# Performance work log

Hardware: AMD Instinct MI355X
Metric: run time of the kernel (lower is better)

Reference implementation:

```python
import jax, jax.numpy as jnp
import numpy as np

EMBED_DIM = 512
BLOCK = 511
N_HEAD = 8
N_GLOBAL = 4
N_LOCAL = 2
N_MIX = 2
RECEP = 4
T = 2 * BLOCK + 2  # [task, clip, BLOCK upper, BLOCK lower]
HD = EMBED_DIM // N_HEAD
NEG = -1e9


def _build_masks():
    bs = BLOCK
    temporal = np.concatenate([np.zeros(2), np.arange(bs) * 2 + 1, np.arange(bs) * 2 + 2])
    seq = temporal[None, :] <= temporal[:, None]  # causal over interleaved temporal order
    tq = np.concatenate([np.arange(bs) * 2 + 1 - 2 * RECEP + 1] * 2)
    tk = np.concatenate([np.arange(bs) * 2 + 1] * 2)
    de = tk[None, :] < tq[:, None]  # keys too far in the past for the sliding window
    local = seq.copy()
    local[2:, 2:] = local[2:, 2:] & ~de
    return jnp.asarray(local), jnp.asarray(seq)


LOCAL_MASK, GLOBAL_MASK = _build_masks()  # (T, T) bool, True = visible


def _linear_params(key, fan_in, fan_out):
    k1, k2 = jax.random.split(key)
    s = 1.0 / np.sqrt(fan_in)
    W = jax.random.uniform(k1, (fan_out, fan_in), minval=-s, maxval=s, dtype=jnp.float32)
    b = jax.random.uniform(k2, (fan_out,), minval=-s, maxval=s, dtype=jnp.float32)
    return W, b


def setup_inputs() -> dict:
    key = jax.random.key(0)
    ks = jax.random.split(key, 10)
    B = 4
    x = jax.random.normal(ks[0], (B, T, EMBED_DIM), dtype=jnp.float32)
    cond_mask = jnp.ones((B, T), dtype=jnp.float32)
    Wq, bq = _linear_params(ks[1], EMBED_DIM, EMBED_DIM)
    Wk, bk = _linear_params(ks[2], EMBED_DIM, EMBED_DIM)
    Wv, bv = _linear_params(ks[3], EMBED_DIM, EMBED_DIM)
    Wqml, bqml = _linear_params(ks[4], EMBED_DIM, HD * N_MIX)
    Wkml, bkml = _linear_params(ks[5], EMBED_DIM, HD * N_MIX)
    Wp, bp = _linear_params(ks[6], EMBED_DIM, EMBED_DIM)
    mix_w = jax.random.normal(ks[7], (N_MIX, 2), dtype=jnp.float32) * 0.5  # Conv2d(2*nm, nm, groups=nm, 1x1)
    bias_clip = jnp.full((1, N_HEAD, 1), 0.5, dtype=jnp.float32)
    bias_clip_ml = jnp.full((1, N_MIX, 1), 0.5, dtype=jnp.float32)
    return dict(x=x, cond_mask=cond_mask, Wq=Wq, bq=bq, Wk=Wk, bk=bk, Wv=Wv, bv=bv,
                Wqml=Wqml, bqml=bqml, Wkml=Wkml, bkml=bkml, mix_w=mix_w, Wp=Wp, bp=bp,
                bias_clip=bias_clip, bias_clip_ml=bias_clip_ml)


def reference(x, cond_mask, Wq, bq, Wk, bk, Wv, bv, Wqml, bqml, Wkml, bkml, mix_w, Wp, bp, bias_clip, bias_clip_ml):
    B, Tx, C = x.shape

    def heads(W, b, nh):
        return (x @ W.T + b).reshape(B, Tx, nh, HD).transpose(0, 2, 1, 3)  # (B, nh, T, hd)

    q = heads(Wq, bq, N_HEAD)
    k = heads(Wk, bk, N_HEAD)
    v = heads(Wv, bv, N_HEAD)
    qml = heads(Wqml, bqml, N_MIX)
    kml = heads(Wkml, bkml, N_MIX)

    scale = 1.0 / np.sqrt(HD)
    # main attention: heads [0:N_LOCAL] local-masked, rest global (causal) masked
    att = jnp.einsum('bhqd,bhkd->bhqk', q, k) * scale
    att = att.at[:, :, :, 1].add(bias_clip)  # learned bias on the CLIP-token key column
    head_mask = jnp.concatenate([
        jnp.broadcast_to(LOCAL_MASK, (N_LOCAL, Tx, Tx)),
        jnp.broadcast_to(GLOBAL_MASK, (N_MIX + N_GLOBAL, Tx, Tx))], axis=0)
    att = jax.nn.softmax(jnp.where(head_mask[None], att, NEG), axis=-1)

    # extra local-masked score maps for the mix heads
    aml = jnp.einsum('bhqd,bhkd->bhqk', qml, kml) * scale
    aml = aml.at[:, :, :, 1].add(bias_clip_ml)
    aml = jax.nn.softmax(jnp.where(LOCAL_MASK[None, None], aml, NEG), axis=-1)

    # grouped 1x1 conv: per mix head, blend (global, local) attention maps
    mix_in = jnp.stack([att[:, N_LOCAL:N_LOCAL + N_MIX], aml], axis=2)  # (B, nm, 2, T, T)
    mix_out = jnp.einsum('ho,bhoqk->bhqk', mix_w, mix_in)

    att_f = jnp.concatenate([att[:, :N_LOCAL], mix_out, att[:, N_LOCAL + N_MIX:]], axis=1)
    y = jnp.einsum('bhqk,bhkd->bhqd', att_f, v)
    y = y.transpose(0, 2, 1, 3).reshape(B, Tx, C)
    return y @ Wp.T + bp
```

## Files before the change

kernel.cpp:

```cpp
#include <hip/hip_runtime.h>

typedef unsigned short u16;
typedef __attribute__((ext_vector_type(8))) __bf16 bf16x8;
typedef __attribute__((ext_vector_type(4))) float f32x4;
typedef __attribute__((ext_vector_type(8))) short short8;
typedef __attribute__((ext_vector_type(4))) u16 us4;
typedef __attribute__((ext_vector_type(4))) unsigned u32x4;

#define T_SEQ 1024
#define PW 1280
#define QSC 0.18033688f
#define L2E 1.4426950408889634f

__device__ __forceinline__ u16 f2bf(float f) {
  unsigned u = __float_as_uint(f);
  u += 0x7fff + ((u >> 16) & 1);
  return (u16)(u >> 16);
}
__device__ __forceinline__ float bf2f(u16 v) {
  return __uint_as_float((unsigned)v << 16);
}

__constant__ u16 GLOB_M[16] = {0x0101,0x0303,0x0707,0x0F0F,0x1F1F,0x3F3F,0x7F7F,0xFFFF,
                               0xFFFF,0x0307,0x070F,0x0F1F,0x1F3F,0x3F7F,0x7FFF,0xFFFF};
__constant__ u16 LOC_M[16]  = {0x0101,0x0303,0x0607,0x0C0D,0x1819,0x3031,0x6061,0xC0C1,
                               0x8183,0x0307,0x060F,0x0C1D,0x1839,0x3071,0x60E1,0xC1C1};

__device__ __forceinline__ void gll16(const u16* gp, u16* lp) {
  __builtin_amdgcn_global_load_lds((const __attribute__((address_space(1))) unsigned*)gp,
                                   (__attribute__((address_space(3))) unsigned*)lp, 16, 0, 0);
}

template<int NISS>
__device__ __forceinline__ void stage_sw(u16* lds, const u16* __restrict__ g,
                                         int ld, int tid) {
  const int w = tid >> 6;
#pragma unroll
  for (int i = 0; i < NISS; ++i) {
    int row = i * 32 + (tid >> 3);
    int cswz = ((tid & 7) << 4) ^ ((row & 7) << 4);
    gll16(g + (size_t)row * ld + (cswz >> 1), lds + i * 2048 + w * 512);
  }
}

__device__ __forceinline__ void stage8(u16* lds, const u16* __restrict__ g,
                                       int ld, int tid) {
  int row = tid >> 3;
  int cswz = (((tid & 7) << 4) ^ ((row & 7) << 4)) >> 1;
  gll16(g + (size_t)row * ld + cswz, lds + (tid >> 6) * 512);
}

__device__ __forceinline__ bf16x8 rd_sw(const u16* lds, int row, int colbyte) {
  return *(const bf16x8*)&lds[row * 64 + ((colbyte ^ ((row & 7) << 4)) >> 1)];
}

__global__ void prep_all(const float4* __restrict__ x, u16* __restrict__ xb,
                         const float* __restrict__ Wq, const float* __restrict__ Wk,
                         const float* __restrict__ Wv, const float* __restrict__ Wqml,
                         const float* __restrict__ Wkml, const float* __restrict__ Wp,
                         const float* __restrict__ bq, const float* __restrict__ bk,
                         const float* __restrict__ bv, const float* __restrict__ bqml,
                         const float* __restrict__ bkml,
                         u16* __restrict__ Wcat, u16* __restrict__ Wpx, float* __restrict__ bcat) {
  if (blockIdx.x < 2048) {
    int i = blockIdx.x * 256 + threadIdx.x;
    float4 v = x[i];
    us4 o = { f2bf(v.x), f2bf(v.y), f2bf(v.z), f2bf(v.w) };
    *(us4*)&xb[i * 4] = o;
    return;
  }
  int idx = (blockIdx.x - 2048) * 256 + threadIdx.x;
  const int NW = 1792 * 512;
  if (idx < NW) {
    int row = idx >> 9;
    float v;
    if (row < 512)       v = Wq[idx];
    else if (row < 1024) v = Wk[idx - 512 * 512];
    else if (row < 1536) v = Wv[idx - 1024 * 512];
    else if (row < 1664) v = Wqml[idx - 1536 * 512];
    else                 v = Wkml[idx - 1664 * 512];
    Wcat[idx] = f2bf(v);
    return;
  }
  int i2 = idx - NW;
  if (i2 < 512 * 640) {
    int n = i2 / 640, k2 = i2 - n * 640;
    float v = (k2 < 512) ? Wp[n * 512 + k2] : Wp[n * 512 + k2 - 384];
    Wpx[i2] = f2bf(v);
    return;
  }
  int i3 = i2 - 512 * 640;
  if (i3 < 1792) {
    float v;
    if (i3 < 512)       v = bq[i3];
    else if (i3 < 1024) v = bk[i3 - 512];
    else if (i3 < 1536) v = bv[i3 - 1024];
    else if (i3 < 1664) v = bqml[i3 - 1536];
    else                v = bkml[i3 - 1664];
    bcat[i3] = v;
  }
}

__global__ __launch_bounds__(256) void gemm_qkv(
    const u16* __restrict__ A, const u16* __restrict__ Bw,
    const float* __restrict__ bias, u16* __restrict__ Pout, u16* __restrict__ Vtb) {
  __shared__ u16 As[2][8192];
  __shared__ u16 Bs[2][8192];
  const int tid = threadIdx.x;
  const int lane = tid & 63, w = tid >> 6;
  const int g = lane >> 4, c = lane & 15;
  const int n0 = blockIdx.x * 128, m0 = blockIdx.y * 128;
  const int wm = (w >> 1) * 64, wn = (w & 1) * 64;

  f32x4 acc[4][4] = {};
  stage_sw<4>(As[0], A + (size_t)m0 * 512, 512, tid);
  stage_sw<4>(Bs[0], Bw + (size_t)n0 * 512, 512, tid);
  __syncthreads();
  for (int ks = 0; ks < 8; ++ks) {
    int cur = ks & 1;
    if (ks + 1 < 8) {
      stage_sw<4>(As[cur ^ 1], A + (size_t)m0 * 512 + (ks + 1) * 64, 512, tid);
      stage_sw<4>(Bs[cur ^ 1], Bw + (size_t)n0 * 512 + (ks + 1) * 64, 512, tid);
    }
#pragma unroll
    for (int h = 0; h < 2; ++h) {
      bf16x8 av[4], bv[4];
#pragma unroll
      for (int f = 0; f < 4; ++f) {
        av[f] = rd_sw(As[cur], wm + f * 16 + c, h * 64 + g * 16);
        bv[f] = rd_sw(Bs[cur], wn + f * 16 + c, h * 64 + g * 16);
      }
#pragma unroll
      for (int fm = 0; fm < 4; ++fm)
#pragma unroll
        for (int fn = 0; fn < 4; ++fn)
          acc[fm][fn] = __builtin_amdgcn_mfma_f32_16x16x32_bf16(av[fm], bv[fn], acc[fm][fn], 0, 0, 0);
    }
    __syncthreads();
  }

  const bool isV = (n0 >= 1024 && n0 < 1536);
#pragma unroll
  for (int fm = 0; fm < 4; ++fm)
#pragma unroll
    for (int fn = 0; fn < 4; ++fn) {
      int row = m0 + wm + fm * 16 + g * 4;
      int col = n0 + wn + fn * 16 + c;
      float bb = bias[col];
      if (isV) {
        int d = col - 1024;
        int bidx = row >> 10, t = row & 1023;
        us4 pack = { f2bf(acc[fm][fn][0] + bb), f2bf(acc[fm][fn][1] + bb),
                     f2bf(acc[fm][fn][2] + bb), f2bf(acc[fm][fn][3] + bb) };
        *(us4*)&Vtb[((size_t)bidx * 512 + d) * 1024 + t] = pack;
      } else {
        float sc = (col < 512 || (col >= 1536 && col < 1664)) ? QSC : 1.0f;
        int pcol = (col < 1024) ? col : col - 512;
#pragma unroll
        for (int r = 0; r < 4; ++r)
          Pout[(size_t)(row + r) * PW + pcol] = f2bf((acc[fm][fn][r] + bb) * sc);
      }
    }
}

__global__ __launch_bounds__(256) void gemm_out(
    const u16* __restrict__ A, const u16* __restrict__ Bw,
    const float* __restrict__ bias, float* __restrict__ Cout) {
  __shared__ u16 As[2][8192];
  __shared__ u16 Bs[2][4096];
  const int tid = threadIdx.x;
  const int lane = tid & 63, w = tid >> 6;
  const int g = lane >> 4, c = lane & 15;
  const int n0 = blockIdx.x * 64, m0 = blockIdx.y * 128;
  const int wm = (w >> 1) * 64, wn = (w & 1) * 32;

  f32x4 acc[4][2] = {};
  stage_sw<4>(As[0], A + (size_t)m0 * 640, 640, tid);
  stage_sw<2>(Bs[0], Bw + (size_t)n0 * 640, 640, tid);
  __syncthreads();
  for (int ks = 0; ks < 10; ++ks) {
    int cur = ks & 1;
    if (ks + 1 < 10) {
      stage_sw<4>(As[cur ^ 1], A + (size_t)m0 * 640 + (ks + 1) * 64, 640, tid);
      stage_sw<2>(Bs[cur ^ 1], Bw + (size_t)n0 * 640 + (ks + 1) * 64, 640, tid);
    }
#pragma unroll
    for (int h = 0; h < 2; ++h) {
      bf16x8 av[4], bv[2];
#pragma unroll
      for (int f = 0; f < 4; ++f)
        av[f] = rd_sw(As[cur], wm + f * 16 + c, h * 64 + g * 16);
#pragma unroll
      for (int f = 0; f < 2; ++f)
        bv[f] = rd_sw(Bs[cur], wn + f * 16 + c, h * 64 + g * 16);
#pragma unroll
      for (int fm = 0; fm < 4; ++fm)
#pragma unroll
        for (int fn = 0; fn < 2; ++fn)
          acc[fm][fn] = __builtin_amdgcn_mfma_f32_16x16x32_bf16(av[fm], bv[fn], acc[fm][fn], 0, 0, 0);
    }
    __syncthreads();
  }
#pragma unroll
  for (int fm = 0; fm < 4; ++fm)
#pragma unroll
    for (int fn = 0; fn < 2; ++fn)
#pragma unroll
      for (int r = 0; r < 4; ++r) {
        int row = m0 + wm + fm * 16 + g * 4 + r;
        int col = n0 + wn + fn * 16 + c;
        Cout[(size_t)row * 512 + col] = acc[fm][fn][r] + bias[col];
      }
}

__global__ __launch_bounds__(512, 4) void attn_k(
    const u16* __restrict__ P, const u16* __restrict__ Vtb,
    u16* __restrict__ Part_o, float* __restrict__ Part_ml,
    const float* __restrict__ bias_clip, const float* __restrict__ bias_clip_ml) {
  __shared__ u16 Ks[2][4096];
  __shared__ u16 Vs[2][4096];
  const int tid = threadIdx.x, lane = tid & 63, w = tid >> 6;
  const int g = lane >> 4, c = lane & 15;
  const int qt2 = blockIdx.x, u = blockIdx.y, b = blockIdx.z;

  int qcol, kcol, vsel;
  bool localMask;
  float kbias;
  unsigned mask;
  unsigned uni = (unsigned)LOC_M[2 * qt2] | (unsigned)LOC_M[2 * qt2 + 1];
  if (u < 24) {
    int h = 2 + (u >> 2), sp = u & 3;
    qcol = h * 64; kcol = 512 + h * 64; vsel = h; kbias = bias_clip[h];
    localMask = false;
    mask = ((unsigned)GLOB_M[2 * qt2] | (unsigned)GLOB_M[2 * qt2 + 1]) & (0x1111u << sp);
  } else if (u < 28) {
    int h = (u - 24) >> 1, sp = (u - 24) & 1;
    qcol = h * 64; kcol = 512 + h * 64; vsel = h; kbias = bias_clip[h];
    localMask = true;
    mask = uni & (sp ? 0xAAAAu : 0x5555u);
  } else {
    int mh = (u - 28) >> 1, sp = (u - 28) & 1;
    qcol = 1024 + mh * 64; kcol = 1152 + mh * 64; vsel = 2 + mh; kbias = bias_clip_ml[mh];
    localMask = true;
    mask = uni & (sp ? 0xAAAAu : 0x5555u);
  }
  kbias *= L2E;
  const size_t baseP = (size_t)b * T_SEQ * PW;
  const u16* __restrict__ Kbase = P + baseP + kcol;
  const u16* __restrict__ Vbase = Vtb + ((size_t)b * 512 + vsel * 64) * 1024;
  const int r0 = qt2 * 128 + w * 16;
  const int qg = r0 + c;

  int tq = (qg < 2) ? 0 : ((qg < 513) ? 2 * qg - 3 : 2 * qg - 1024);
  int upmax = (tq - 1) >> 1;
  int lomax = (tq - 2) >> 1;
  int wmin = (localMask && qg >= 2) ? ((qg < 513 ? qg - 2 : qg - 513) - 3) : -1000000;

  float mM = -1e8f, lL = 0.0f;
  f32x4 o[4] = {};

  if (mask) {
    bf16x8 aq0 = *(const bf16x8*)&P[baseP + (size_t)qg * PW + qcol + g * 8];
    bf16x8 aq1 = *(const bf16x8*)&P[baseP + (size_t)qg * PW + qcol + 32 + g * 8];

    const int nt = __popc(mask);
    int kts[4] = {0, 0, 0, 0};
    unsigned rem = mask;
#pragma unroll
    for (int j = 0; j < 4; ++j) {
      if (j < nt) { kts[j] = __ffs(rem) - 1; rem &= rem - 1; }
    }
    stage8(Ks[0], Kbase + (size_t)(kts[0] * 64) * PW, PW, tid);
    stage8(Vs[0], Vbase + kts[0] * 64, 1024, tid);
    if (nt > 1) {
      stage8(Ks[1], Kbase + (size_t)(kts[1] * 64) * PW, PW, tid);
      stage8(Vs[1], Vbase + kts[1] * 64, 1024, tid);
    }

#pragma unroll
    for (int j = 0; j < 4; ++j) {
      if (j >= nt) break;
      const int sl = j & 1;
      if (j < nt - 1) asm volatile("s_waitcnt vmcnt(2)" ::: "memory");
      else            asm volatile("s_waitcnt vmcnt(0)" ::: "memory");
      __builtin_amdgcn_sched_barrier(0);
      __builtin_amdgcn_s_barrier();

      const int k0 = kts[j] * 64;

      float s[4][4];
      __builtin_amdgcn_s_setprio(1);
#pragma unroll
      for (int cb = 0; cb < 4; ++cb) {
        f32x4 accs = {};
        bf16x8 bk0 = rd_sw(Ks[sl], cb * 16 + c, g * 16);
        bf16x8 bk1 = rd_sw(Ks[sl], cb * 16 + c, 64 + g * 16);
        accs = __builtin_amdgcn_mfma_f32_16x16x32_bf16(bk0, aq0, accs, 0, 0, 0);
        accs = __builtin_amdgcn_mfma_f32_16x16x32_bf16(bk1, aq1, accs, 0, 0, 0);
#pragma unroll
        for (int r = 0; r < 4; ++r) s[cb][r] = accs[r];
      }
      __builtin_amdgcn_s_setprio(0);

#pragma unroll
      for (int cb = 0; cb < 4; ++cb) {
        int kb = k0 + cb * 16 + g * 4;
#pragma unroll
        for (int r = 0; r < 4; ++r) {
          int kk = kb + r;
          bool tok = kk < 2;
          bool low = kk >= 513;
          int jk = kk - (low ? 513 : 2);
          int bnd = low ? lomax : upmax;
          bool vis = tok | ((jk <= bnd) & (jk >= wmin));
          float addb = (kk == 1) ? kbias : 0.0f;
          s[cb][r] = vis ? (s[cb][r] + addb) : -1e9f;
        }
      }

      float rmax = s[0][0];
#pragma unroll
      for (int cb = 0; cb < 4; ++cb)
#pragma unroll
        for (int r = 0; r < 4; ++r) rmax = fmaxf(rmax, s[cb][r]);
      rmax = fmaxf(rmax, __shfl_xor(rmax, 16));
      rmax = fmaxf(rmax, __shfl_xor(rmax, 32));
      float mnew = fmaxf(mM, rmax);
      float fr = exp2f(mM - mnew);
      float psum = 0.0f;
#pragma unroll
      for (int cb = 0; cb < 4; ++cb)
#pragma unroll
        for (int r = 0; r < 4; ++r) {
          float p = exp2f(s[cb][r] - mnew);
          s[cb][r] = p;
          psum += p;
        }
      psum += __shfl_xor(psum, 16);
      psum += __shfl_xor(psum, 32);
      lL = lL * fr + psum;
      mM = mnew;
#pragma unroll
      for (int db = 0; db < 4; ++db) o[db] *= fr;

      unsigned wpk[4][2];
#pragma unroll
      for (int cb = 0; cb < 4; ++cb) {
        asm("v_cvt_pk_bf16_f32 %0, %1, %2" : "=v"(wpk[cb][0]) : "v"(s[cb][0]), "v"(s[cb][1]));
        asm("v_cvt_pk_bf16_f32 %0, %1, %2" : "=v"(wpk[cb][1]) : "v"(s[cb][2]), "v"(s[cb][3]));
      }
#pragma unroll
      for (int ks2 = 0; ks2 < 2; ++ks2) {
        unsigned tw[4];
#pragma unroll
        for (int rr = 0; rr < 2; ++rr) {
          unsigned L = wpk[2 * ks2][rr], H = wpk[2 * ks2 + 1][rr];
          unsigned sA = (g & 1) ? L : H;
          unsigned sB = (g & 1) ? H : L;
          unsigned X16 = (unsigned)__shfl_xor((int)sA, 16);
          unsigned X32 = (unsigned)__shfl_xor((int)sA, 32);
          unsigned X48 = (unsigned)__shfl_xor((int)sB, 48);
          unsigned a  = (g >= 2) ? ((g == 3) ? X16 : X32) : ((g == 1) ? X48 : L);
          unsigned b2 = (g >= 2) ? ((g == 3) ? H : X48) : ((g == 1) ? X32 : X16);
          tw[rr] = a; tw[2 + rr] = b2;
        }
        u32x4 tw4 = { tw[0], tw[1], tw[2], tw[3] };
        bf16x8 ap = __builtin_bit_cast(bf16x8, tw4);
        __builtin_amdgcn_s_setprio(1);
#pragma unroll
        for (int db = 0; db < 4; ++db) {
          bf16x8 av = rd_sw(Vs[sl], db * 16 + c, ks2 * 64 + g * 16);
          o[db] = __builtin_amdgcn_mfma_f32_16x16x32_bf16(av, ap, o[db], 0, 0, 0);
        }
        __builtin_amdgcn_s_setprio(0);
      }

      __builtin_amdgcn_s_barrier();
      if (j + 2 < nt) {
        stage8(Ks[sl], Kbase + (size_t)(kts[j + 2] * 64) * PW, PW, tid);
        stage8(Vs[sl], Vbase + kts[j + 2] * 64, 1024, tid);
      }
    }
  }

  u16* po = Part_o + ((size_t)(u * 4 + b)) * T_SEQ * 64;
#pragma unroll
  for (int db = 0; db < 4; ++db) {
    us4 pk = { f2bf(o[db][0]), f2bf(o[db][1]), f2bf(o[db][2]), f2bf(o[db][3]) };
    *(us4*)&po[(size_t)qg * 64 + db * 16 + g * 4] = pk;
  }
  if (g == 0) {
    float2 ml = { mM, lL };
    *(float2*)&Part_ml[(((size_t)(u * 4 + b)) * T_SEQ + qg) * 2] = ml;
  }
}

__global__ __launch_bounds__(256) void combine_k(
    const u16* __restrict__ Part_o, const float* __restrict__ Part_ml,
    u16* __restrict__ Y, const float* __restrict__ mix_w) {
  int idx = blockIdx.x * 256 + threadIdx.x;
  int q4 = idx & 15;
  int row = (idx >> 4) & 1023;
  int bb = (idx >> 14) & 3;
  int j = idx >> 16;
  int ns, bs, outcol;
  float wgt;
  if (j < 6)      { ns = 4; bs = j * 4;            outcol = 128 + j * 64;       wgt = (j < 2) ? mix_w[2 * j] : 1.0f; }
  else if (j < 8) { ns = 2; bs = 24 + (j - 6) * 2; outcol = (j - 6) * 64;       wgt = 1.0f; }
  else            { ns = 2; bs = 28 + (j - 8) * 2; outcol = 512 + (j - 8) * 64; wgt = mix_w[(j - 8) * 2 + 1]; }

  float mv[4], lv[4];
  float ms = -1e30f;
  for (int s = 0; s < ns; ++s) {
    size_t base = (((size_t)(bs + s) * 4 + bb) * 1024 + row) * 2;
    mv[s] = Part_ml[base];
    lv[s] = Part_ml[base + 1];
    ms = fmaxf(ms, mv[s]);
  }
  float denom = 0.0f, e[4];
  for (int s = 0; s < ns; ++s) { e[s] = exp2f(mv[s] - ms); denom += lv[s] * e[s]; }
  float inv = wgt / denom;
  float out[4] = {0.f, 0.f, 0.f, 0.f};
  for (int s = 0; s < ns; ++s) {
    us4 ov = *(const us4*)&Part_o[(((size_t)(bs + s) * 4 + bb) * 1024 + row) * 64 + q4 * 4];
#pragma unroll
    for (int t = 0; t < 4; ++t) out[t] += e[s] * bf2f(ov[t]);
  }
  us4 pk = { f2bf(out[0] * inv), f2bf(out[1] * inv), f2bf(out[2] * inv), f2bf(out[3] * inv) };
  *(us4*)&Y[((size_t)bb * 1024 + row) * 640 + outcol + q4 * 4] = pk;
}

extern "C" void kernel_launch(void* const* d_in, const int* in_sizes, int n_in,
                              void* d_out, int out_size, void* d_ws, size_t ws_size,
                              hipStream_t stream) {
  const float* x     = (const float*)d_in[0];
  const float* Wq    = (const float*)d_in[2];
  const float* bq    = (const float*)d_in[3];
  const float* Wk    = (const float*)d_in[4];
  const float* bk    = (const float*)d_in[5];
  const float* Wv    = (const float*)d_in[6];
  const float* bv    = (const float*)d_in[7];
  const float* Wqml  = (const float*)d_in[8];
  const float* bqml  = (const float*)d_in[9];
  const float* Wkml  = (const float*)d_in[10];
  const float* bkml  = (const float*)d_in[11];
  const float* mixw  = (const float*)d_in[12];
  const float* Wp    = (const float*)d_in[13];
  const float* bp    = (const float*)d_in[14];
  const float* bclip = (const float*)d_in[15];
  const float* bclipml = (const float*)d_in[16];

  u16* xb   = (u16*)d_ws;
  u16* Wcat = xb + 4096 * 512;
  u16* Wpx  = Wcat + 1792 * 512;
  u16* Ybuf = Wpx + 512 * 640;
  u16* Vtb  = Ybuf + 4096 * 640;
  u16* Pbuf = Vtb + 4 * 512 * 1024;
  float* bcat = (float*)(Pbuf + 4096 * 1280);
  u16* Part_o = (u16*)(bcat + 2048);
  float* Part_ml = (float*)(Part_o + 32 * 4 * 1024 * 64);

  prep_all<<<6919, 256, 0, stream>>>((const float4*)x, xb, Wq, Wk, Wv, Wqml, Wkml, Wp,
                                     bq, bk, bv, bqml, bkml, Wcat, Wpx, bcat);
  gemm_qkv<<<dim3(14, 32), 256, 0, stream>>>(xb, Wcat, bcat, Pbuf, Vtb);
  attn_k<<<dim3(8, 32, 4), 512, 0, stream>>>(Pbuf, Vtb, Part_o, Part_ml, bclip, bclipml);
  combine_k<<<2560, 256, 0, stream>>>(Part_o, Part_ml, Ybuf, mixw);
  gemm_out<<<dim3(8, 32), 256, 0, stream>>>(Ybuf, Wpx, bp, (float*)d_out);
}
```

Measured before the change: 76.97 us.

## Halve attention key-split factor and use 8 waves in QKV GEMM

```diff
diff --git a/kernel.cpp b/kernel.cpp
--- a/kernel.cpp
+++ b/kernel.cpp
@@ -29,6 +29,16 @@
 __device__ __forceinline__ void gll16(const u16* gp, u16* lp) {
   __builtin_amdgcn_global_load_lds((const __attribute__((address_space(1))) unsigned*)gp,
                                    (__attribute__((address_space(3))) unsigned*)lp, 16, 0, 0);
+}
+
+__device__ __forceinline__ void stage512(u16* lds, const u16* __restrict__ g,
+                                         int ld, int tid) {
+#pragma unroll
+  for (int i = 0; i < 2; ++i) {
+    int row = i * 64 + (tid >> 3);
+    int cswz = ((tid & 7) << 4) ^ ((row & 7) << 4);
+    gll16(g + (size_t)row * ld + (cswz >> 1), lds + i * 4096 + (tid >> 6) * 512);
+  }
 }
 
 template<int NISS>
@@ -101,7 +111,7 @@
   }
 }
 
-__global__ __launch_bounds__(256) void gemm_qkv(
+__global__ __launch_bounds__(512) void gemm_qkv(
     const u16* __restrict__ A, const u16* __restrict__ Bw,
     const float* __restrict__ bias, u16* __restrict__ Pout, u16* __restrict__ Vtb) {
   __shared__ u16 As[2][8192];
@@ -110,30 +120,31 @@
   const int lane = tid & 63, w = tid >> 6;
   const int g = lane >> 4, c = lane & 15;
   const int n0 = blockIdx.x * 128, m0 = blockIdx.y * 128;
-  const int wm = (w >> 1) * 64, wn = (w & 1) * 64;
-
-  f32x4 acc[4][4] = {};
-  stage_sw<4>(As[0], A + (size_t)m0 * 512, 512, tid);
-  stage_sw<4>(Bs[0], Bw + (size_t)n0 * 512, 512, tid);
+  const int wm = (w >> 2) * 64, wn = (w & 3) * 32;
+
+  f32x4 acc[4][2] = {};
+  stage512(As[0], A + (size_t)m0 * 512, 512, tid);
+  stage512(Bs[0], Bw + (size_t)n0 * 512, 512, tid);
   __syncthreads();
   for (int ks = 0; ks < 8; ++ks) {
     int cur = ks & 1;
     if (ks + 1 < 8) {
-      stage_sw<4>(As[cur ^ 1], A + (size_t)m0 * 512 + (ks + 1) * 64, 512, tid);
-      stage_sw<4>(Bs[cur ^ 1], Bw + (size_t)n0 * 512 + (ks + 1) * 64, 512, tid);
+      stage512(As[cur ^ 1], A + (size_t)m0 * 512 + (ks + 1) * 64, 512, tid);
+      stage512(Bs[cur ^ 1], Bw + (size_t)n0 * 512 + (ks + 1) * 64, 512, tid);
     }
 #pragma unroll
     for (int h = 0; h < 2; ++h) {
-      bf16x8 av[4], bv[4];
-#pragma unroll
-      for (int f = 0; f < 4; ++f) {
+      bf16x8 av[4], bv[2];
+#pragma unroll
+      for (int f = 0; f < 4; ++f)
         av[f] = rd_sw(As[cur], wm + f * 16 + c, h * 64 + g * 16);
+#pragma unroll
+      for (int f = 0; f < 2; ++f)
         bv[f] = rd_sw(Bs[cur], wn + f * 16 + c, h * 64 + g * 16);
-      }
 #pragma unroll
       for (int fm = 0; fm < 4; ++fm)
 #pragma unroll
-        for (int fn = 0; fn < 4; ++fn)
+        for (int fn = 0; fn < 2; ++fn)
           acc[fm][fn] = __builtin_amdgcn_mfma_f32_16x16x32_bf16(av[fm], bv[fn], acc[fm][fn], 0, 0, 0);
     }
     __syncthreads();
@@ -143,7 +154,7 @@
 #pragma unroll
   for (int fm = 0; fm < 4; ++fm)
 #pragma unroll
-    for (int fn = 0; fn < 4; ++fn) {
+    for (int fn = 0; fn < 2; ++fn) {
       int row = m0 + wm + fm * 16 + g * 4;
       int col = n0 + wn + fn * 16 + c;
       float bb = bias[col];
@@ -227,22 +238,22 @@
   bool localMask;
   float kbias;
   unsigned mask;
-  unsigned uni = (unsigned)LOC_M[2 * qt2] | (unsigned)LOC_M[2 * qt2 + 1];
-  if (u < 24) {
-    int h = 2 + (u >> 2), sp = u & 3;
+  unsigned uniL = (unsigned)LOC_M[2 * qt2] | (unsigned)LOC_M[2 * qt2 + 1];
+  if (u < 12) {
+    int h = 2 + (u >> 1), sp = u & 1;
     qcol = h * 64; kcol = 512 + h * 64; vsel = h; kbias = bias_clip[h];
     localMask = false;
-    mask = ((unsigned)GLOB_M[2 * qt2] | (unsigned)GLOB_M[2 * qt2 + 1]) & (0x1111u << sp);
-  } else if (u < 28) {
-    int h = (u - 24) >> 1, sp = (u - 24) & 1;
+    mask = ((unsigned)GLOB_M[2 * qt2] | (unsigned)GLOB_M[2 * qt2 + 1]) & (sp ? 0xAAAAu : 0x5555u);
+  } else if (u < 14) {
+    int h = u - 12;
     qcol = h * 64; kcol = 512 + h * 64; vsel = h; kbias = bias_clip[h];
     localMask = true;
-    mask = uni & (sp ? 0xAAAAu : 0x5555u);
+    mask = uniL;
   } else {
-    int mh = (u - 28) >> 1, sp = (u - 28) & 1;
+    int mh = u - 14;
     qcol = 1024 + mh * 64; kcol = 1152 + mh * 64; vsel = 2 + mh; kbias = bias_clip_ml[mh];
     localMask = true;
-    mask = uni & (sp ? 0xAAAAu : 0x5555u);
+    mask = uniL;
   }
   kbias *= L2E;
   const size_t baseP = (size_t)b * T_SEQ * PW;
@@ -263,30 +274,25 @@
     bf16x8 aq0 = *(const bf16x8*)&P[baseP + (size_t)qg * PW + qcol + g * 8];
     bf16x8 aq1 = *(const bf16x8*)&P[baseP + (size_t)qg * PW + qcol + 32 + g * 8];
 
-    const int nt = __popc(mask);
-    int kts[4] = {0, 0, 0, 0};
     unsigned rem = mask;
-#pragma unroll
-    for (int j = 0; j < 4; ++j) {
-      if (j < nt) { kts[j] = __ffs(rem) - 1; rem &= rem - 1; }
-    }
-    stage8(Ks[0], Kbase + (size_t)(kts[0] * 64) * PW, PW, tid);
-    stage8(Vs[0], Vbase + kts[0] * 64, 1024, tid);
-    if (nt > 1) {
-      stage8(Ks[1], Kbase + (size_t)(kts[1] * 64) * PW, PW, tid);
-      stage8(Vs[1], Vbase + kts[1] * 64, 1024, tid);
-    }
-
-#pragma unroll
-    for (int j = 0; j < 4; ++j) {
-      if (j >= nt) break;
-      const int sl = j & 1;
-      if (j < nt - 1) asm volatile("s_waitcnt vmcnt(2)" ::: "memory");
+    int kt_cur = __ffs(rem) - 1; rem &= rem - 1;
+    int kt_n1 = -1;
+    stage8(Ks[0], Kbase + (size_t)(kt_cur * 64) * PW, PW, tid);
+    stage8(Vs[0], Vbase + kt_cur * 64, 1024, tid);
+    if (rem) {
+      kt_n1 = __ffs(rem) - 1; rem &= rem - 1;
+      stage8(Ks[1], Kbase + (size_t)(kt_n1 * 64) * PW, PW, tid);
+      stage8(Vs[1], Vbase + kt_n1 * 64, 1024, tid);
+    }
+    int sl = 0;
+
+    for (;;) {
+      if (kt_n1 >= 0) asm volatile("s_waitcnt vmcnt(2)" ::: "memory");
       else            asm volatile("s_waitcnt vmcnt(0)" ::: "memory");
       __builtin_amdgcn_sched_barrier(0);
       __builtin_amdgcn_s_barrier();
 
-      const int k0 = kts[j] * 64;
+      const int k0 = kt_cur * 64;
 
       float s[4][4];
       __builtin_amdgcn_s_setprio(1);
@@ -376,10 +382,14 @@
       }
 
       __builtin_amdgcn_s_barrier();
-      if (j + 2 < nt) {
-        stage8(Ks[sl], Kbase + (size_t)(kts[j + 2] * 64) * PW, PW, tid);
-        stage8(Vs[sl], Vbase + kts[j + 2] * 64, 1024, tid);
-      }
+      int kt_n2 = -1;
+      if (rem) {
+        kt_n2 = __ffs(rem) - 1; rem &= rem - 1;
+        stage8(Ks[sl], Kbase + (size_t)(kt_n2 * 64) * PW, PW, tid);
+        stage8(Vs[sl], Vbase + kt_n2 * 64, 1024, tid);
+      }
+      if (kt_n1 < 0) break;
+      kt_cur = kt_n1; kt_n1 = kt_n2; sl ^= 1;
     }
   }
 
@@ -405,11 +415,11 @@
   int j = idx >> 16;
   int ns, bs, outcol;
   float wgt;
-  if (j < 6)      { ns = 4; bs = j * 4;            outcol = 128 + j * 64;       wgt = (j < 2) ? mix_w[2 * j] : 1.0f; }
-  else if (j < 8) { ns = 2; bs = 24 + (j - 6) * 2; outcol = (j - 6) * 64;       wgt = 1.0f; }
-  else            { ns = 2; bs = 28 + (j - 8) * 2; outcol = 512 + (j - 8) * 64; wgt = mix_w[(j - 8) * 2 + 1]; }
-
-  float mv[4], lv[4];
+  if (j < 6)      { ns = 2; bs = j * 2;       outcol = 128 + j * 64;       wgt = (j < 2) ? mix_w[2 * j] : 1.0f; }
+  else if (j < 8) { ns = 1; bs = 12 + (j - 6); outcol = (j - 6) * 64;       wgt = 1.0f; }
+  else            { ns = 1; bs = 14 + (j - 8); outcol = 512 + (j - 8) * 64; wgt = mix_w[(j - 8) * 2 + 1]; }
+
+  float mv[2], lv[2];
   float ms = -1e30f;
   for (int s = 0; s < ns; ++s) {
     size_t base = (((size_t)(bs + s) * 4 + bb) * 1024 + row) * 2;
@@ -417,7 +427,7 @@
     lv[s] = Part_ml[base + 1];
     ms = fmaxf(ms, mv[s]);
   }
-  float denom = 0.0f, e[4];
+  float denom = 0.0f, e[2];
   for (int s = 0; s < ns; ++s) { e[s] = exp2f(mv[s] - ms); denom += lv[s] * e[s]; }
   float inv = wgt / denom;
   float out[4] = {0.f, 0.f, 0.f, 0.f};
@@ -458,12 +468,12 @@
   u16* Pbuf = Vtb + 4 * 512 * 1024;
   float* bcat = (float*)(Pbuf + 4096 * 1280);
   u16* Part_o = (u16*)(bcat + 2048);
-  float* Part_ml = (float*)(Part_o + 32 * 4 * 1024 * 64);
+  float* Part_ml = (float*)(Part_o + 16 * 4 * 1024 * 64);
 
   prep_all<<<6919, 256, 0, stream>>>((const float4*)x, xb, Wq, Wk, Wv, Wqml, Wkml, Wp,
                                      bq, bk, bv, bqml, bkml, Wcat, Wpx, bcat);
-  gemm_qkv<<<dim3(14, 32), 256, 0, stream>>>(xb, Wcat, bcat, Pbuf, Vtb);
-  attn_k<<<dim3(8, 32, 4), 512, 0, stream>>>(Pbuf, Vtb, Part_o, Part_ml, bclip, bclipml);
+  gemm_qkv<<<dim3(14, 32), 512, 0, stream>>>(xb, Wcat, bcat, Pbuf, Vtb);
+  attn_k<<<dim3(8, 16, 4), 512, 0, stream>>>(Pbuf, Vtb, Part_o, Part_ml, bclip, bclipml);
   combine_k<<<2560, 256, 0, stream>>>(Part_o, Part_ml, Ybuf, mixw);
   gemm_out<<<dim3(8, 32), 256, 0, stream>>>(Ybuf, Wpx, bp, (float*)d_out);
 }
```

Measured after the change: 75.45 us, median of 2. 2.0% less time.
